# Performance work log

Hardware: AMD Instinct MI355X
Metric: run time of the kernel (lower is better)

Reference implementation:

```python
import jax, jax.numpy as jnp
import numpy as np

B, Q, K, H, DQ, DK, DV = 8, 256, 256, 256, 256, 256, 256


def setup_inputs() -> dict:
    key = jax.random.key(0)
    k1, k2, k3, k4, k5, k6, k7 = jax.random.split(key, 7)
    queries = jax.random.normal(k1, (B, Q, DQ), dtype=jnp.float32)
    keys = jax.random.normal(k2, (B, K, DK), dtype=jnp.float32)
    values = jax.random.normal(k3, (B, K, DV), dtype=jnp.float32)
    valid_lens = jax.random.randint(k4, (B,), 1, K + 1)
    # learned params (torch Linear without bias); stored as (in, out)
    s = 1.0 / np.sqrt(H)
    W_q = jax.random.uniform(k5, (DQ, H), minval=-s, maxval=s, dtype=jnp.float32)
    W_k = jax.random.uniform(k6, (DK, H), minval=-s, maxval=s, dtype=jnp.float32)
    w_v = jax.random.uniform(k7, (H,), minval=-s, maxval=s, dtype=jnp.float32)
    return {"queries": queries, "keys": keys, "values": values,
            "valid_lens": valid_lens, "W_q": W_q, "W_k": W_k, "w_v": w_v}


def reference(queries, keys, values, valid_lens, W_q, W_k, w_v):
    q = queries @ W_q                      # (B, Q, H)
    k = keys @ W_k                         # (B, K, H)
    # broadcast add + tanh -> (B, Q, K, H), then linear score -> (B, Q, K)
    features = jnp.tanh(q[:, :, None, :] + k[:, None, :, :])
    scores = jnp.einsum('bqkh,h->bqk', features, w_v)
    mask = jnp.arange(K)[None, None, :] >= valid_lens[:, None, None]  # (B,1,K)
    scores = jnp.where(mask, -1000000.0, scores)
    attn = jax.nn.softmax(scores, axis=-1)  # (B, Q, K)
    return jnp.einsum('bqk,bkd->bqd', attn, values)  # (B, Q, DV)
```

## Files before the change

kernel.cpp:

```cpp
#include <hip/hip_runtime.h>
#include <hip/hip_bf16.h>

#define LOG2E 1.4426950408889634f
#define C2    (2.0f * LOG2E)

static __device__ __forceinline__ float fast_exp2(float x) {
#if __has_builtin(__builtin_amdgcn_exp2f)
  return __builtin_amdgcn_exp2f(x);
#else
  return exp2f(x);
#endif
}
static __device__ __forceinline__ float fast_rcp(float x) {
#if __has_builtin(__builtin_amdgcn_rcpf)
  return __builtin_amdgcn_rcpf(x);
#else
  return 1.0f / x;
#endif
}

typedef short bf16x8 __attribute__((ext_vector_type(8)));
typedef float f32x4  __attribute__((ext_vector_type(4)));

static __device__ __forceinline__ short f2bf(float x) {
  unsigned u = __float_as_uint(x);
  u += 0x7fff + ((u >> 16) & 1);
  return (short)(u >> 16);
}

__global__ __launch_bounds__(256, 4) void proj_kernel(
    const float* __restrict__ queries, const float* __restrict__ keys,
    const float* __restrict__ W_q,     const float* __restrict__ W_k,
    const int*   __restrict__ vlen,
    float* __restrict__ qs, float* __restrict__ ks_p)
{
  const int bz = blockIdx.z;
  const float* X = bz ? keys : queries;
  const float* W = bz ? W_k  : W_q;
  const int n0 = blockIdx.x * 16;
  const int m0 = blockIdx.y * 64;

  if (bz == 1) {
    const int vl = vlen[m0 >> 8];
    if ((m0 & 255) >= vl) return;
  }

  const int t = threadIdx.x;
  const int l = t & 63;
  const int w = t >> 6;

  __shared__ short Wp[8 * 64 * 8];

  {
    const int krow = t >> 2, nseg = t & 3;
#pragma unroll
    for (int p = 0; p < 4; ++p) {
      const int k = p * 64 + krow;
      float4 v = *(const float4*)&W[k * 256 + n0 + nseg * 4];
      const int kc = k >> 5, grp = (k & 31) >> 3, j = k & 7;
      const int lbase = grp * 16 + nseg * 4;
      Wp[(kc * 64 + lbase + 0) * 8 + j] = f2bf(v.x);
      Wp[(kc * 64 + lbase + 1) * 8 + j] = f2bf(v.y);
      Wp[(kc * 64 + lbase + 2) * 8 + j] = f2bf(v.z);
      Wp[(kc * 64 + lbase + 3) * 8 + j] = f2bf(v.w);
    }
  }
  __syncthreads();

  const int mb   = m0 + w * 16;
  const int row  = mb + (l & 15);
  const int kofs = (l >> 4) * 8;

  f32x4 acc = {0.f, 0.f, 0.f, 0.f};
#pragma unroll
  for (int kc = 0; kc < 8; ++kc) {
    float4 a0 = *(const float4*)&X[(size_t)row * 256 + kc * 32 + kofs];
    float4 a1 = *(const float4*)&X[(size_t)row * 256 + kc * 32 + kofs + 4];
    bf16x8 af;
    af[0] = f2bf(a0.x); af[1] = f2bf(a0.y); af[2] = f2bf(a0.z); af[3] = f2bf(a0.w);
    af[4] = f2bf(a1.x); af[5] = f2bf(a1.y); af[6] = f2bf(a1.z); af[7] = f2bf(a1.w);
    bf16x8 bfv = *(bf16x8*)&Wp[(kc * 64 + l) * 8];
    acc = __builtin_amdgcn_mfma_f32_16x16x32_bf16(af, bfv, acc, 0, 0, 0);
  }

  const int c = l & 15;
#pragma unroll
  for (int j = 0; j < 4; ++j) {
    const int rj = (l >> 4) * 4 + j;
    const float o = fast_exp2(acc[j] * C2);
    if (bz == 0) {
      qs[(size_t)(mb + rj) * 256 + n0 + c] = o;
    } else {
      const int b  = mb >> 8;
      const int kl = (mb & 255) + rj;
      ks_p[((size_t)(b * 64 + ((n0 + c) >> 2)) * 256 + kl) * 4 + (c & 3)] = o;
    }
  }
}

#define SC_STEP(c)                                                         \
  sc[j][0] = fmaf(wv.c, fast_rcp(fmaf(qv0.c, kv[j].c, 1.f)), sc[j][0]);    \
  sc[j][1] = fmaf(wv.c, fast_rcp(fmaf(qv1.c, kv[j].c, 1.f)), sc[j][1]);    \
  sc[j][2] = fmaf(wv.c, fast_rcp(fmaf(qv2.c, kv[j].c, 1.f)), sc[j][2]);    \
  sc[j][3] = fmaf(wv.c, fast_rcp(fmaf(qv3.c, kv[j].c, 1.f)), sc[j][3]);

template <int NJ>
__device__ __forceinline__ void score_loop(
    const float* __restrict__ kp,
    const float* __restrict__ qp,
    const float* __restrict__ wvp, int h4b, float (&sc)[4][4])
{
#pragma unroll 2
  for (int h4 = h4b; h4 < h4b + 8; ++h4) {
    float4 kv[NJ];
#pragma unroll
    for (int j = 0; j < NJ; ++j)
      kv[j] = *(const float4*)(kp + h4 * 1024 + j * 256);
    float4 qv0 = *(const float4*)(qp + 0 * 256 + h4 * 4);
    float4 qv1 = *(const float4*)(qp + 1 * 256 + h4 * 4);
    float4 qv2 = *(const float4*)(qp + 2 * 256 + h4 * 4);
    float4 qv3 = *(const float4*)(qp + 3 * 256 + h4 * 4);
    float4 wv  = *(const float4*)(wvp + h4 * 4);
#pragma unroll
    for (int j = 0; j < NJ; ++j) {
      SC_STEP(x); SC_STEP(y); SC_STEP(z); SC_STEP(w);
    }
  }
}

__global__ __launch_bounds__(512, 4) void attn_kernel(
    const float* __restrict__ qs, const float* __restrict__ ks_p,
    const float* __restrict__ values, const int* __restrict__ vlen,
    const float* __restrict__ w_v, float* __restrict__ out)
{
  const int t    = threadIdx.x;
  const int lane = t & 63;
  const int w    = t >> 6;
  const int bx   = blockIdx.x;
  const int b    = ((bx & 7) + (bx >> 6)) & 7;
  const int q0   = (bx >> 3) * 4;

  __shared__ __align__(16) float sbuf[8192];
  __shared__ __align__(16) float p2[256 * 4];
  __shared__ float rsum_lds[4];

  const int vl = vlen[b];
  const int nj = (vl + 63) >> 6;

  float s0 = w_v[lane] + w_v[lane + 64] + w_v[lane + 128] + w_v[lane + 192];
#pragma unroll
  for (int off = 32; off; off >>= 1) s0 += __shfl_xor(s0, off);
  const float Wsum = s0;

  const float* qp = qs + (size_t)(b * 256 + q0) * 256;
  const float* kp = ks_p + (size_t)b * 65536 + lane * 4;
  const int h4b = w * 8;

  float sc[4][4] = {};
  switch (nj) {
    case 1:  score_loop<1>(kp, qp, w_v, h4b, sc); break;
    case 2:  score_loop<2>(kp, qp, w_v, h4b, sc); break;
    case 3:  score_loop<3>(kp, qp, w_v, h4b, sc); break;
    default: score_loop<4>(kp, qp, w_v, h4b, sc); break;
  }

#pragma unroll
  for (int j = 0; j < 4; ++j)
    *(float4*)&sbuf[((w * 4 + j) * 64 + lane) * 4] =
        make_float4(sc[j][0], sc[j][1], sc[j][2], sc[j][3]);
  __syncthreads();

  if (w < 4) {
    const int q = w;
    float scores[4];
    float mx = -3.4e38f;
#pragma unroll 4
    for (int j = 0; j < nj; ++j) {
      float s = 0.f;
#pragma unroll
      for (int ww = 0; ww < 8; ++ww)
        s += sbuf[((ww * 4 + j) * 64 + lane) * 4 + q];
      float v = Wsum - 2.f * s;
      if (j * 64 + lane >= vl) v = -1000000.0f;
      scores[j] = v;
      mx = fmaxf(mx, v);
    }
#pragma unroll
    for (int off = 32; off; off >>= 1) mx = fmaxf(mx, __shfl_xor(mx, off));
    float sum = 0.f;
#pragma unroll 4
    for (int j = 0; j < nj; ++j) {
      float p = fast_exp2((scores[j] - mx) * LOG2E);
      p2[(j * 64 + lane) * 4 + q] = p;
      sum += p;
    }
#pragma unroll
    for (int off = 32; off; off >>= 1) sum += __shfl_xor(sum, off);
    if (lane == 0) rsum_lds[q] = sum;
  }
  __syncthreads();

  float4 acc[4];
#pragma unroll
  for (int q = 0; q < 4; ++q) acc[q] = make_float4(0.f, 0.f, 0.f, 0.f);
  const float* Vb = values + (size_t)b * 65536 + lane * 4;
  if (w < vl) {
    float4 v = *(const float4*)(Vb + (size_t)w * 256);
    for (int k = w; k < vl; k += 8) {
      float4 vn = v;
      if (k + 8 < vl) vn = *(const float4*)(Vb + (size_t)(k + 8) * 256);
      float4 pk = *(const float4*)&p2[k * 4];
      acc[0].x = fmaf(pk.x, v.x, acc[0].x);
      acc[0].y = fmaf(pk.x, v.y, acc[0].y);
      acc[0].z = fmaf(pk.x, v.z, acc[0].z);
      acc[0].w = fmaf(pk.x, v.w, acc[0].w);
      acc[1].x = fmaf(pk.y, v.x, acc[1].x);
      acc[1].y = fmaf(pk.y, v.y, acc[1].y);
      acc[1].z = fmaf(pk.y, v.z, acc[1].z);
      acc[1].w = fmaf(pk.y, v.w, acc[1].w);
      acc[2].x = fmaf(pk.z, v.x, acc[2].x);
      acc[2].y = fmaf(pk.z, v.y, acc[2].y);
      acc[2].z = fmaf(pk.z, v.z, acc[2].z);
      acc[2].w = fmaf(pk.z, v.w, acc[2].w);
      acc[3].x = fmaf(pk.w, v.x, acc[3].x);
      acc[3].y = fmaf(pk.w, v.y, acc[3].y);
      acc[3].z = fmaf(pk.w, v.z, acc[3].z);
      acc[3].w = fmaf(pk.w, v.w, acc[3].w);
      v = vn;
    }
  }
#pragma unroll
  for (int q = 0; q < 4; ++q)
    *(float4*)&sbuf[(w * 4 + q) * 256 + lane * 4] = acc[q];
  __syncthreads();

#pragma unroll
  for (int rep = 0; rep < 2; ++rep) {
    int o = t + rep * 512;
    int q = o >> 8, d = o & 255;
    float s = 0.f;
#pragma unroll
    for (int ww = 0; ww < 8; ++ww) s += sbuf[(ww * 4 + q) * 256 + d];
    out[(size_t)(b * 256 + q0 + q) * 256 + d] = s * fast_rcp(rsum_lds[q]);
  }
}

extern "C" void kernel_launch(void* const* d_in, const int* in_sizes, int n_in,
                              void* d_out, int out_size, void* d_ws, size_t ws_size,
                              hipStream_t stream) {
  const float* queries = (const float*)d_in[0];
  const float* keys    = (const float*)d_in[1];
  const float* values  = (const float*)d_in[2];
  const int*   vlenp   = (const int*)d_in[3];
  const float* W_q     = (const float*)d_in[4];
  const float* W_k     = (const float*)d_in[5];
  const float* w_v     = (const float*)d_in[6];
  float* out = (float*)d_out;

  float* qs   = (float*)d_ws;
  float* ks_p = qs + 2048 * 256;

  dim3 pgrid(16, 32, 2);
  proj_kernel<<<pgrid, 256, 0, stream>>>(queries, keys, W_q, W_k, vlenp, qs, ks_p);
  attn_kernel<<<512, 512, 0, stream>>>(qs, ks_p, values, vlenp, w_v, out);
}
```

Before: 38.98 us.

## Stage key-projection chunks through double-buffered LDS in the score phase

The score loop now prefetches the next chunk of projected keys into registers and writes it into a double-buffered LDS region, while it computes on the current chunk read back from LDS. A block barrier follows each of the 8 chunks. The head-dimension assignment is interleaved across waves (h4 = c*8 + w) instead of contiguous per wave. The aim is to hide global-load latency, but each wave reads only its own slice, so nothing is shared across waves. The cost is extra LDS traffic, 8 barriers, and a larger LDS footprint (about 70 KB per block) that can cut resident blocks per CU.

```diff
diff --git a/kernel.cpp b/kernel.cpp
--- a/kernel.cpp
+++ b/kernel.cpp
@@ -105,26 +105,60 @@
   sc[j][3] = fmaf(wv.c, fast_rcp(fmaf(qv3.c, kv[j].c, 1.f)), sc[j][3]);
 
 template <int NJ>
-__device__ __forceinline__ void score_loop(
-    const float* __restrict__ kp,
+__device__ __forceinline__ void score_phase(
+    const float* __restrict__ kp_b,
     const float* __restrict__ qp,
-    const float* __restrict__ wvp, int h4b, float (&sc)[4][4])
+    const float* __restrict__ wvp,
+    const int lane, const int w, float* __restrict__ lds,
+    float (&sc)[4][4])
 {
-#pragma unroll 2
-  for (int h4 = h4b; h4 < h4b + 8; ++h4) {
-    float4 kv[NJ];
-#pragma unroll
-    for (int j = 0; j < NJ; ++j)
-      kv[j] = *(const float4*)(kp + h4 * 1024 + j * 256);
+  float* const buf0 = lds;
+  float* const buf1 = lds + NJ * 2048;
+  const int rbase = (w * NJ) * 256 + lane * 4;
+
+  {
+    const float* src = kp_b + (size_t)w * 1024 + lane * 4;
+#pragma unroll
+    for (int j = 0; j < NJ; ++j) {
+      float4 r = *(const float4*)(src + j * 256);
+      *(float4*)&buf0[rbase + j * 256] = r;
+    }
+  }
+  __syncthreads();
+
+#pragma unroll
+  for (int c = 0; c < 8; ++c) {
+    float* const bufc = (c & 1) ? buf1 : buf0;
+    float* const bufn = (c & 1) ? buf0 : buf1;
+
+    float4 nxt[NJ];
+    if (c < 7) {
+      const float* src = kp_b + (size_t)((c + 1) * 8 + w) * 1024 + lane * 4;
+#pragma unroll
+      for (int j = 0; j < NJ; ++j) nxt[j] = *(const float4*)(src + j * 256);
+    }
+
+    const int h4 = c * 8 + w;
     float4 qv0 = *(const float4*)(qp + 0 * 256 + h4 * 4);
     float4 qv1 = *(const float4*)(qp + 1 * 256 + h4 * 4);
     float4 qv2 = *(const float4*)(qp + 2 * 256 + h4 * 4);
     float4 qv3 = *(const float4*)(qp + 3 * 256 + h4 * 4);
     float4 wv  = *(const float4*)(wvp + h4 * 4);
+    float4 kv[NJ];
+#pragma unroll
+    for (int j = 0; j < NJ; ++j)
+      kv[j] = *(const float4*)&bufc[rbase + j * 256];
 #pragma unroll
     for (int j = 0; j < NJ; ++j) {
       SC_STEP(x); SC_STEP(y); SC_STEP(z); SC_STEP(w);
     }
+
+    if (c < 7) {
+#pragma unroll
+      for (int j = 0; j < NJ; ++j)
+        *(float4*)&bufn[rbase + j * 256] = nxt[j];
+    }
+    __syncthreads();
   }
 }
 
@@ -140,9 +174,10 @@
   const int b    = ((bx & 7) + (bx >> 6)) & 7;
   const int q0   = (bx >> 3) * 4;
 
-  __shared__ __align__(16) float sbuf[8192];
-  __shared__ __align__(16) float p2[256 * 4];
-  __shared__ float rsum_lds[4];
+  __shared__ __align__(16) float lds[16384 + 1024 + 16];
+  float* const sbuf = lds;
+  float* const p2   = lds + 16384;
+  float* const rsum_lds = lds + 17408;
 
   const int vl = vlen[b];
   const int nj = (vl + 63) >> 6;
@@ -152,16 +187,15 @@
   for (int off = 32; off; off >>= 1) s0 += __shfl_xor(s0, off);
   const float Wsum = s0;
 
-  const float* qp = qs + (size_t)(b * 256 + q0) * 256;
-  const float* kp = ks_p + (size_t)b * 65536 + lane * 4;
-  const int h4b = w * 8;
+  const float* qp   = qs + (size_t)(b * 256 + q0) * 256;
+  const float* kp_b = ks_p + (size_t)b * 65536;
 
   float sc[4][4] = {};
   switch (nj) {
-    case 1:  score_loop<1>(kp, qp, w_v, h4b, sc); break;
-    case 2:  score_loop<2>(kp, qp, w_v, h4b, sc); break;
-    case 3:  score_loop<3>(kp, qp, w_v, h4b, sc); break;
-    default: score_loop<4>(kp, qp, w_v, h4b, sc); break;
+    case 1:  score_phase<1>(kp_b, qp, w_v, lane, w, lds, sc); break;
+    case 2:  score_phase<2>(kp_b, qp, w_v, lane, w, lds, sc); break;
+    case 3:  score_phase<3>(kp_b, qp, w_v, lane, w, lds, sc); break;
+    default: score_phase<4>(kp_b, qp, w_v, lane, w, lds, sc); break;
   }
 
 #pragma unroll
```

Measured after the change: 78.57 us. 102% more time.

## Split attention over key chunks with partial numerators and a finalize kernel

Applied to the files above, without the earlier changes.

Replaces the single attention kernel with a split-K scheme. Each block handles one 64-key chunk for four queries and skips chunks past the valid length, which spreads work more evenly across blocks. Each block writes an unnormalized fp16 numerator and an fp32 denominator, and a new finalize kernel sums the chunks and normalizes. Projected keys are now stored in bf16 to halve that traffic. The change drops the max subtraction in softmax, relying on scores staying bounded, and adds a third launch plus partial-result traffic through workspace memory.

```diff
diff --git a/kernel.cpp b/kernel.cpp
--- a/kernel.cpp
+++ b/kernel.cpp
@@ -1,5 +1,6 @@
 #include <hip/hip_runtime.h>
 #include <hip/hip_bf16.h>
+#include <hip/hip_fp16.h>
 
 #define LOG2E 1.4426950408889634f
 #define C2    (2.0f * LOG2E)
@@ -27,12 +28,15 @@
   u += 0x7fff + ((u >> 16) & 1);
   return (short)(u >> 16);
 }
+static __device__ __forceinline__ float bf2f(unsigned short u) {
+  return __uint_as_float((unsigned)u << 16);
+}
 
 __global__ __launch_bounds__(256, 4) void proj_kernel(
     const float* __restrict__ queries, const float* __restrict__ keys,
     const float* __restrict__ W_q,     const float* __restrict__ W_k,
     const int*   __restrict__ vlen,
-    float* __restrict__ qs, float* __restrict__ ks_p)
+    float* __restrict__ qs, unsigned short* __restrict__ ks_pb)
 {
   const int bz = blockIdx.z;
   const float* X = bz ? keys : queries;
@@ -93,156 +97,161 @@
     } else {
       const int b  = mb >> 8;
       const int kl = (mb & 255) + rj;
-      ks_p[((size_t)(b * 64 + ((n0 + c) >> 2)) * 256 + kl) * 4 + (c & 3)] = o;
+      ks_pb[((size_t)(b * 64 + ((n0 + c) >> 2)) * 256 + kl) * 4 + (c & 3)] =
+          (unsigned short)f2bf(o);
     }
   }
 }
 
-#define SC_STEP(c)                                                         \
-  sc[j][0] = fmaf(wv.c, fast_rcp(fmaf(qv0.c, kv[j].c, 1.f)), sc[j][0]);    \
-  sc[j][1] = fmaf(wv.c, fast_rcp(fmaf(qv1.c, kv[j].c, 1.f)), sc[j][1]);    \
-  sc[j][2] = fmaf(wv.c, fast_rcp(fmaf(qv2.c, kv[j].c, 1.f)), sc[j][2]);    \
-  sc[j][3] = fmaf(wv.c, fast_rcp(fmaf(qv3.c, kv[j].c, 1.f)), sc[j][3]);
-
-template <int NJ>
-__device__ __forceinline__ void score_loop(
-    const float* __restrict__ kp,
-    const float* __restrict__ qp,
-    const float* __restrict__ wvp, int h4b, float (&sc)[4][4])
+__global__ __launch_bounds__(256, 8) void scorepv_kernel(
+    const float* __restrict__ qs, const unsigned short* __restrict__ ks_pb,
+    const float* __restrict__ values, const int* __restrict__ vlen,
+    const float* __restrict__ w_v,
+    __half* __restrict__ numer, float* __restrict__ denom)
 {
-#pragma unroll 2
-  for (int h4 = h4b; h4 < h4b + 8; ++h4) {
-    float4 kv[NJ];
-#pragma unroll
-    for (int j = 0; j < NJ; ++j)
-      kv[j] = *(const float4*)(kp + h4 * 1024 + j * 256);
+  const unsigned u  = blockIdx.x;
+  const int hi = u >> 8;
+  const int c  = (int)(u ^ hi) & 3;
+  const int b  = (((int)(u >> 2) & 7) + hi) & 7;
+  const int g  = (int)(u >> 5) & 63;
+
+  const int vl = vlen[b];
+  const int nj = (vl + 63) >> 6;
+  if (c >= nj) return;
+
+  const int t    = threadIdx.x;
+  const int lane = t & 63;
+  const int w    = t >> 6;
+
+  __shared__ __align__(16) float sbuf[4 * 64 * 4];
+  __shared__ __align__(16) float p2[64 * 4];
+  __shared__ __align__(16) float pbuf[4 * 4 * 256];
+
+  float s0 = w_v[lane] + w_v[lane + 64] + w_v[lane + 128] + w_v[lane + 192];
+#pragma unroll
+  for (int off = 32; off; off >>= 1) s0 += __shfl_xor(s0, off);
+  const float Wsum = s0;
+
+  const float* qp = qs + (size_t)(b * 256 + g * 4) * 256;
+  const int k = c * 64 + lane;
+  const unsigned short* kp = ks_pb + ((size_t)b * 64 * 256 + k) * 4;
+
+  float sc[4] = {0.f, 0.f, 0.f, 0.f};
+#pragma unroll 4
+  for (int h4 = w * 16; h4 < w * 16 + 16; ++h4) {
+    ushort4 kb = *(const ushort4*)(kp + (size_t)h4 * 1024);
+    const float kx = bf2f(kb.x), ky = bf2f(kb.y),
+                kz = bf2f(kb.z), kw = bf2f(kb.w);
     float4 qv0 = *(const float4*)(qp + 0 * 256 + h4 * 4);
     float4 qv1 = *(const float4*)(qp + 1 * 256 + h4 * 4);
     float4 qv2 = *(const float4*)(qp + 2 * 256 + h4 * 4);
     float4 qv3 = *(const float4*)(qp + 3 * 256 + h4 * 4);
-    float4 wv  = *(const float4*)(wvp + h4 * 4);
-#pragma unroll
-    for (int j = 0; j < NJ; ++j) {
-      SC_STEP(x); SC_STEP(y); SC_STEP(z); SC_STEP(w);
+    float4 wv  = *(const float4*)(w_v + h4 * 4);
+    sc[0] = fmaf(wv.x, fast_rcp(fmaf(qv0.x, kx, 1.f)), sc[0]);
+    sc[1] = fmaf(wv.x, fast_rcp(fmaf(qv1.x, kx, 1.f)), sc[1]);
+    sc[2] = fmaf(wv.x, fast_rcp(fmaf(qv2.x, kx, 1.f)), sc[2]);
+    sc[3] = fmaf(wv.x, fast_rcp(fmaf(qv3.x, kx, 1.f)), sc[3]);
+    sc[0] = fmaf(wv.y, fast_rcp(fmaf(qv0.y, ky, 1.f)), sc[0]);
+    sc[1] = fmaf(wv.y, fast_rcp(fmaf(qv1.y, ky, 1.f)), sc[1]);
+    sc[2] = fmaf(wv.y, fast_rcp(fmaf(qv2.y, ky, 1.f)), sc[2]);
+    sc[3] = fmaf(wv.y, fast_rcp(fmaf(qv3.y, ky, 1.f)), sc[3]);
+    sc[0] = fmaf(wv.z, fast_rcp(fmaf(qv0.z, kz, 1.f)), sc[0]);
+    sc[1] = fmaf(wv.z, fast_rcp(fmaf(qv1.z, kz, 1.f)), sc[1]);
+    sc[2] = fmaf(wv.z, fast_rcp(fmaf(qv2.z, kz, 1.f)), sc[2]);
+    sc[3] = fmaf(wv.z, fast_rcp(fmaf(qv3.z, kz, 1.f)), sc[3]);
+    sc[0] = fmaf(wv.w, fast_rcp(fmaf(qv0.w, kw, 1.f)), sc[0]);
+    sc[1] = fmaf(wv.w, fast_rcp(fmaf(qv1.w, kw, 1.f)), sc[1]);
+    sc[2] = fmaf(wv.w, fast_rcp(fmaf(qv2.w, kw, 1.f)), sc[2]);
+    sc[3] = fmaf(wv.w, fast_rcp(fmaf(qv3.w, kw, 1.f)), sc[3]);
+  }
+  *(float4*)&sbuf[(w * 64 + lane) * 4] = make_float4(sc[0], sc[1], sc[2], sc[3]);
+  __syncthreads();
+
+  {
+    float s = sbuf[(0 * 64 + lane) * 4 + w] + sbuf[(1 * 64 + lane) * 4 + w] +
+              sbuf[(2 * 64 + lane) * 4 + w] + sbuf[(3 * 64 + lane) * 4 + w];
+    float v = Wsum - 2.f * s;
+    float p = (k < vl) ? fast_exp2(v * LOG2E) : 0.f;
+    p2[lane * 4 + w] = p;
+    float ps = p;
+#pragma unroll
+    for (int off = 32; off; off >>= 1) ps += __shfl_xor(ps, off);
+    if (lane == 0) denom[(size_t)c * 2048 + b * 256 + g * 4 + w] = ps;
+  }
+  __syncthreads();
+
+  const int nk = min(64, vl - c * 64);
+  float4 acc[4];
+#pragma unroll
+  for (int q = 0; q < 4; ++q) acc[q] = make_float4(0.f, 0.f, 0.f, 0.f);
+  const float* Vb = values + (size_t)(b * 256 + c * 64) * 256 + lane * 4;
+  for (int kk = w; kk < nk; kk += 4) {
+    float4 p4 = *(const float4*)&p2[kk * 4];
+    float4 vv = *(const float4*)(Vb + (size_t)kk * 256);
+    acc[0].x = fmaf(p4.x, vv.x, acc[0].x);
+    acc[0].y = fmaf(p4.x, vv.y, acc[0].y);
+    acc[0].z = fmaf(p4.x, vv.z, acc[0].z);
+    acc[0].w = fmaf(p4.x, vv.w, acc[0].w);
+    acc[1].x = fmaf(p4.y, vv.x, acc[1].x);
+    acc[1].y = fmaf(p4.y, vv.y, acc[1].y);
+    acc[1].z = fmaf(p4.y, vv.z, acc[1].z);
+    acc[1].w = fmaf(p4.y, vv.w, acc[1].w);
+    acc[2].x = fmaf(p4.z, vv.x, acc[2].x);
+    acc[2].y = fmaf(p4.z, vv.y, acc[2].y);
+    acc[2].z = fmaf(p4.z, vv.z, acc[2].z);
+    acc[2].w = fmaf(p4.z, vv.w, acc[2].w);
+    acc[3].x = fmaf(p4.w, vv.x, acc[3].x);
+    acc[3].y = fmaf(p4.w, vv.y, acc[3].y);
+    acc[3].z = fmaf(p4.w, vv.z, acc[3].z);
+    acc[3].w = fmaf(p4.w, vv.w, acc[3].w);
+  }
+#pragma unroll
+  for (int q = 0; q < 4; ++q)
+    *(float4*)&pbuf[(w * 4 + q) * 256 + lane * 4] = acc[q];
+  __syncthreads();
+
+  {
+    const int q = t >> 6, d0 = (t & 63) * 4;
+    float4 s4 = make_float4(0.f, 0.f, 0.f, 0.f);
+#pragma unroll
+    for (int ww = 0; ww < 4; ++ww) {
+      float4 v = *(const float4*)&pbuf[(ww * 4 + q) * 256 + d0];
+      s4.x += v.x; s4.y += v.y; s4.z += v.z; s4.w += v.w;
     }
-  }
-}
-
-__global__ __launch_bounds__(512, 4) void attn_kernel(
-    const float* __restrict__ qs, const float* __restrict__ ks_p,
-    const float* __restrict__ values, const int* __restrict__ vlen,
-    const float* __restrict__ w_v, float* __restrict__ out)
+    __half* np = numer + ((size_t)c * 2048 + b * 256 + g * 4 + q) * 256 + d0;
+    short4 st;
+    st.x = (short)__half_as_ushort(__float2half(s4.x));
+    st.y = (short)__half_as_ushort(__float2half(s4.y));
+    st.z = (short)__half_as_ushort(__float2half(s4.z));
+    st.w = (short)__half_as_ushort(__float2half(s4.w));
+    *(short4*)np = st;
+  }
+}
+
+__global__ __launch_bounds__(256) void finalize_kernel(
+    const __half* __restrict__ numer, const float* __restrict__ denom,
+    const int* __restrict__ vlen, float* __restrict__ out)
 {
-  const int t    = threadIdx.x;
-  const int lane = t & 63;
-  const int w    = t >> 6;
-  const int bx   = blockIdx.x;
-  const int b    = ((bx & 7) + (bx >> 6)) & 7;
-  const int q0   = (bx >> 3) * 4;
-
-  __shared__ __align__(16) float sbuf[8192];
-  __shared__ __align__(16) float p2[256 * 4];
-  __shared__ float rsum_lds[4];
-
-  const int vl = vlen[b];
-  const int nj = (vl + 63) >> 6;
-
-  float s0 = w_v[lane] + w_v[lane + 64] + w_v[lane + 128] + w_v[lane + 192];
-#pragma unroll
-  for (int off = 32; off; off >>= 1) s0 += __shfl_xor(s0, off);
-  const float Wsum = s0;
-
-  const float* qp = qs + (size_t)(b * 256 + q0) * 256;
-  const float* kp = ks_p + (size_t)b * 65536 + lane * 4;
-  const int h4b = w * 8;
-
-  float sc[4][4] = {};
-  switch (nj) {
-    case 1:  score_loop<1>(kp, qp, w_v, h4b, sc); break;
-    case 2:  score_loop<2>(kp, qp, w_v, h4b, sc); break;
-    case 3:  score_loop<3>(kp, qp, w_v, h4b, sc); break;
-    default: score_loop<4>(kp, qp, w_v, h4b, sc); break;
-  }
-
-#pragma unroll
-  for (int j = 0; j < 4; ++j)
-    *(float4*)&sbuf[((w * 4 + j) * 64 + lane) * 4] =
-        make_float4(sc[j][0], sc[j][1], sc[j][2], sc[j][3]);
-  __syncthreads();
-
-  if (w < 4) {
-    const int q = w;
-    float scores[4];
-    float mx = -3.4e38f;
+  const int t  = threadIdx.x;
+  const int r  = blockIdx.x * 4 + (t >> 6);
+  const int d0 = (t & 63) * 4;
+  const int b  = r >> 8;
+  const int nj = (vlen[b] + 63) >> 6;
+
+  float den = 0.f;
+  float4 s = make_float4(0.f, 0.f, 0.f, 0.f);
 #pragma unroll 4
-    for (int j = 0; j < nj; ++j) {
-      float s = 0.f;
-#pragma unroll
-      for (int ww = 0; ww < 8; ++ww)
-        s += sbuf[((ww * 4 + j) * 64 + lane) * 4 + q];
-      float v = Wsum - 2.f * s;
-      if (j * 64 + lane >= vl) v = -1000000.0f;
-      scores[j] = v;
-      mx = fmaxf(mx, v);
-    }
-#pragma unroll
-    for (int off = 32; off; off >>= 1) mx = fmaxf(mx, __shfl_xor(mx, off));
-    float sum = 0.f;
-#pragma unroll 4
-    for (int j = 0; j < nj; ++j) {
-      float p = fast_exp2((scores[j] - mx) * LOG2E);
-      p2[(j * 64 + lane) * 4 + q] = p;
-      sum += p;
-    }
-#pragma unroll
-    for (int off = 32; off; off >>= 1) sum += __shfl_xor(sum, off);
-    if (lane == 0) rsum_lds[q] = sum;
-  }
-  __syncthreads();
-
-  float4 acc[4];
-#pragma unroll
-  for (int q = 0; q < 4; ++q) acc[q] = make_float4(0.f, 0.f, 0.f, 0.f);
-  const float* Vb = values + (size_t)b * 65536 + lane * 4;
-  if (w < vl) {
-    float4 v = *(const float4*)(Vb + (size_t)w * 256);
-    for (int k = w; k < vl; k += 8) {
-      float4 vn = v;
-      if (k + 8 < vl) vn = *(const float4*)(Vb + (size_t)(k + 8) * 256);
-      float4 pk = *(const float4*)&p2[k * 4];
-      acc[0].x = fmaf(pk.x, v.x, acc[0].x);
-      acc[0].y = fmaf(pk.x, v.y, acc[0].y);
-      acc[0].z = fmaf(pk.x, v.z, acc[0].z);
-      acc[0].w = fmaf(pk.x, v.w, acc[0].w);
-      acc[1].x = fmaf(pk.y, v.x, acc[1].x);
-      acc[1].y = fmaf(pk.y, v.y, acc[1].y);
-      acc[1].z = fmaf(pk.y, v.z, acc[1].z);
-      acc[1].w = fmaf(pk.y, v.w, acc[1].w);
-      acc[2].x = fmaf(pk.z, v.x, acc[2].x);
-      acc[2].y = fmaf(pk.z, v.y, acc[2].y);
-      acc[2].z = fmaf(pk.z, v.z, acc[2].z);
-      acc[2].w = fmaf(pk.z, v.w, acc[2].w);
-      acc[3].x = fmaf(pk.w, v.x, acc[3].x);
-      acc[3].y = fmaf(pk.w, v.y, acc[3].y);
-      acc[3].z = fmaf(pk.w, v.z, acc[3].z);
-      acc[3].w = fmaf(pk.w, v.w, acc[3].w);
-      v = vn;
-    }
-  }
-#pragma unroll
-  for (int q = 0; q < 4; ++q)
-    *(float4*)&sbuf[(w * 4 + q) * 256 + lane * 4] = acc[q];
-  __syncthreads();
-
-#pragma unroll
-  for (int rep = 0; rep < 2; ++rep) {
-    int o = t + rep * 512;
-    int q = o >> 8, d = o & 255;
-    float s = 0.f;
-#pragma unroll
-    for (int ww = 0; ww < 8; ++ww) s += sbuf[(ww * 4 + q) * 256 + d];
-    out[(size_t)(b * 256 + q0 + q) * 256 + d] = s * fast_rcp(rsum_lds[q]);
-  }
+  for (int c = 0; c < nj; ++c) {
+    den += denom[(size_t)c * 2048 + r];
+    ushort4 nv = *(const ushort4*)(numer + ((size_t)c * 2048 + r) * 256 + d0);
+    s.x += __half2float(__ushort_as_half(nv.x));
+    s.y += __half2float(__ushort_as_half(nv.y));
+    s.z += __half2float(__ushort_as_half(nv.z));
+    s.w += __half2float(__ushort_as_half(nv.w));
+  }
+  const float rin = fast_rcp(den);
+  *(float4*)&out[(size_t)r * 256 + d0] =
+      make_float4(s.x * rin, s.y * rin, s.z * rin, s.w * rin);
 }
 
 extern "C" void kernel_launch(void* const* d_in, const int* in_sizes, int n_in,
@@ -257,10 +266,14 @@
   const float* w_v     = (const float*)d_in[6];
   float* out = (float*)d_out;
 
-  float* qs   = (float*)d_ws;
-  float* ks_p = qs + 2048 * 256;
+  float*          qs    = (float*)d_ws;
+  unsigned short* ks_pb = (unsigned short*)((char*)d_ws + ((size_t)2 << 20));
+  __half* numer = (__half*)((char*)d_ws + ((size_t)3 << 20));
+  float*  denom = (float*)((char*)d_ws + ((size_t)7 << 20));
 
   dim3 pgrid(16, 32, 2);
-  proj_kernel<<<pgrid, 256, 0, stream>>>(queries, keys, W_q, W_k, vlenp, qs, ks_p);
-  attn_kernel<<<512, 512, 0, stream>>>(qs, ks_p, values, vlenp, w_v, out);
-}
+  proj_kernel<<<pgrid, 256, 0, stream>>>(queries, keys, W_q, W_k, vlenp, qs, ks_pb);
+  scorepv_kernel<<<2048, 256, 0, stream>>>(qs, ks_pb, values, vlenp, w_v,
+                                           numer, denom);
+  finalize_kernel<<<512, 256, 0, stream>>>(numer, denom, vlenp, out);
+}
```

After: 46.46 us. 19.2% more time.
